# Kernel optimization log

Measured on AMD Instinct MI355X. Metric: run time of the kernel, lower is better.

The kernel has to match this reference:

```python
import jax, jax.numpy as jnp
import numpy as np
import math

HIDDEN = 1024
HEADS = 16

def setup_inputs() -> dict:
    key = jax.random.key(0)
    k1, k2, k3 = jax.random.split(key, 3)
    B, T, C = 4, 2048, HIDDEN
    x = jax.random.normal(k1, (B, T, C), dtype=jnp.float32)
    w_qkv = jax.random.normal(k2, (C, 3 * C), dtype=jnp.float32) * (1.0 / math.sqrt(C))
    b_qkv = jnp.zeros((3 * C,), dtype=jnp.float32)
    w_out = jax.random.normal(k3, (C, C), dtype=jnp.float32) * (1.0 / math.sqrt(C))
    b_out = jnp.zeros((C,), dtype=jnp.float32)
    return {"x": x, "w_qkv": w_qkv, "b_qkv": b_qkv, "w_out": w_out, "b_out": b_out}

def reference(x, w_qkv, b_qkv, w_out, b_out):
    B, T, C = x.shape
    H = HEADS
    D = C // H  # head dim
    qkv = x @ w_qkv + b_qkv  # [B,T,3C]
    q, k, v = jnp.split(qkv, 3, axis=2)
    # [B,T,C] -> [B,H,T,D]
    q = q.reshape(B, T, H, D).transpose(0, 2, 1, 3)
    k = k.reshape(B, T, H, D).transpose(0, 2, 1, 3)
    v = v.reshape(B, T, H, D).transpose(0, 2, 1, 3)
    scale = 1.0 / math.sqrt(D)
    logits = jnp.einsum('bhqd,bhkd->bhqk', q, k) * scale  # [B,H,T,T]
    causal = jnp.tril(jnp.ones((T, T), dtype=bool))
    logits = jnp.where(causal[None, None, :, :], logits, -jnp.inf)
    probs = jax.nn.softmax(logits, axis=-1)
    out = jnp.einsum('bhqk,bhkd->bhqd', probs, v)  # [B,H,T,D]
    out = out.transpose(0, 2, 1, 3).reshape(B, T, C)
    return out @ w_out + b_out
```

## Files before the change

kernel.cpp:

```cpp
#include <hip/hip_runtime.h>
#include <hip/hip_bf16.h>

#define C_DIM  1024
#define NHEAD  16
#define DHEAD  64
#define T_LEN  2048
#define B_SZ   4
#define M_ROWS (B_SZ * T_LEN)
#define QKV_N  (3 * C_DIM)

typedef __bf16 bf16x8 __attribute__((ext_vector_type(8)));
typedef float  f32x4  __attribute__((ext_vector_type(4)));
typedef unsigned short ushort8_t __attribute__((ext_vector_type(8)));
typedef unsigned int   uint4_t   __attribute__((ext_vector_type(4)));
typedef short          short4_t  __attribute__((ext_vector_type(4)));

#if __has_builtin(__builtin_amdgcn_mfma_f32_16x16x16bf16_1k)
#define HAVE_MFMA_X16 1
#else
#define HAVE_MFMA_X16 0
#endif

__device__ __forceinline__ unsigned short f2bf(float f) {
    union { float f; unsigned int u; } v; v.f = f;
    unsigned int r = v.u + 0x7FFFu + ((v.u >> 16) & 1u);
    return (unsigned short)(r >> 16);
}

__device__ __forceinline__ bf16x8 as_bf16x8(ushort8_t u) {
    return __builtin_bit_cast(bf16x8, u);
}

__device__ __forceinline__ f32x4 mfma16(bf16x8 a, bf16x8 b, f32x4 c) {
    return __builtin_amdgcn_mfma_f32_16x16x32_bf16(a, b, c, 0, 0, 0);
}

#define GLL16(gsrc, ldst) __builtin_amdgcn_global_load_lds( \
    (const __attribute__((address_space(1))) void*)(gsrc),  \
    (__attribute__((address_space(3))) void*)(ldst), 16, 0, 0)

__device__ __forceinline__ int xcd_remap(int id, int nwg) {
    const int q = nwg >> 3, r = nwg & 7;
    const int xcd = id & 7, off = id >> 3;
    return (xcd < r) ? (xcd * (q + 1) + off) : (r * (q + 1) + (xcd - r) * q + off);
}

__global__ void k_convert(const float* __restrict__ in, unsigned short* __restrict__ out, int n4) {
    int i = blockIdx.x * blockDim.x + threadIdx.x;
    if (i >= n4) return;
    const float4 v = ((const float4*)in)[i];
    unsigned int lo = (unsigned int)f2bf(v.x) | ((unsigned int)f2bf(v.y) << 16);
    unsigned int hi = (unsigned int)f2bf(v.z) | ((unsigned int)f2bf(v.w) << 16);
    ((uint2*)out)[i] = make_uint2(lo, hi);
}

__global__ void k_transpose_bf16(const float* __restrict__ w, unsigned short* __restrict__ wT,
                                 int K, int N) {
    __shared__ float tile[32][33];
    const int n0 = blockIdx.x * 32, k0 = blockIdx.y * 32;
    const int tx = threadIdx.x, ty = threadIdx.y;
    for (int i = 0; i < 32; i += 8)
        tile[ty + i][tx] = w[(size_t)(k0 + ty + i) * N + (n0 + tx)];
    __syncthreads();
    for (int i = 0; i < 32; i += 8)
        wT[(size_t)(n0 + ty + i) * K + (k0 + tx)] = f2bf(tile[tx][ty + i]);
}

__global__ void k_transpose_v(const unsigned short* __restrict__ qkv,
                              unsigned short* __restrict__ vtg) {
    __shared__ unsigned short tile[32][33];
    const int tt = blockIdx.x;
    const int dy = blockIdx.y;
    const int bh = dy >> 1, dtile = dy & 1;
    const int b = bh >> 4, h = bh & 15;
    const int t0 = tt * 32, d0 = dtile * 32;
    const int tx = threadIdx.x, ty = threadIdx.y;
    const unsigned short* src = qkv + (size_t)b * T_LEN * QKV_N + 2 * C_DIM + h * DHEAD + d0;
    for (int i = 0; i < 32; i += 8)
        tile[ty + i][tx] = src[(size_t)(t0 + ty + i) * QKV_N + tx];
    __syncthreads();
    unsigned short* dst = vtg + ((size_t)bh * DHEAD + d0) * T_LEN + t0;
    for (int i = 0; i < 32; i += 8)
        dst[(size_t)(ty + i) * T_LEN + tx] = tile[tx][ty + i];
}

template<int BF16_OUT>
__global__ __launch_bounds__(256) void k_gemm(const unsigned short* __restrict__ A,
                       const unsigned short* __restrict__ Bt,
                       const float* __restrict__ bias,
                       void* __restrict__ C,
                       unsigned short* __restrict__ vtg,
                       int M, int N, int K) {
    __shared__ unsigned short As[128][64];
    __shared__ unsigned short Bs[128][64];

    const int tid  = threadIdx.x;
    const int lane = tid & 63;
    const int wv   = tid >> 6;
    const int wm = wv >> 1, wn = wv & 1;

    const int nwg = gridDim.x * gridDim.y;
    const int wg  = xcd_remap(blockIdx.y * gridDim.x + blockIdx.x, nwg);
    const int bx = wg % gridDim.x, by = wg / gridDim.x;
    const int m0 = by * 128;
    const int n0 = bx * 128;
    const int lr = lane & 15, lg = lane >> 4;

    f32x4 acc[4][4];
#pragma unroll
    for (int i = 0; i < 4; i++)
#pragma unroll
        for (int j = 0; j < 4; j++) acc[i][j] = (f32x4){0.f, 0.f, 0.f, 0.f};

    const int gr = lane >> 3;
    const int gc = 8 * ((lane & 7) ^ gr);

    for (int kt = 0; kt < K; kt += 64) {
        __syncthreads();
#pragma unroll
        for (int j = 0; j < 4; j++) {
            const int row = 32 * wv + 8 * j;
            GLL16(A  + (size_t)(m0 + row + gr) * K + kt + gc, &As[row][0]);
            GLL16(Bt + (size_t)(n0 + row + gr) * K + kt + gc, &Bs[row][0]);
        }
        __syncthreads();

#pragma unroll
        for (int s = 0; s < 2; s++) {
            const int cb = (s * 64 + lg * 16) ^ ((lr & 7) << 4);
            bf16x8 af[4], bfr[4];
#pragma unroll
            for (int i = 0; i < 4; i++)
                af[i] = as_bf16x8(*(const ushort8_t*)((const char*)&As[wm * 64 + i * 16 + lr][0] + cb));
#pragma unroll
            for (int j = 0; j < 4; j++)
                bfr[j] = as_bf16x8(*(const ushort8_t*)((const char*)&Bs[wn * 64 + j * 16 + lr][0] + cb));
#pragma unroll
            for (int i = 0; i < 4; i++)
#pragma unroll
                for (int j = 0; j < 4; j++)
                    acc[i][j] = mfma16(af[i], bfr[j], acc[i][j]);
        }
    }

    const bool isV = (vtg != nullptr) && (n0 >= 2 * C_DIM);
#pragma unroll
    for (int i = 0; i < 4; i++) {
#pragma unroll
        for (int j = 0; j < 4; j++) {
            const int col = n0 + wn * 64 + j * 16 + lr;
            const float bv = bias ? bias[col] : 0.f;
            if (isV) {
                const int dcol = col - 2 * C_DIM;
                const int hh = dcol >> 6, dd = dcol & 63;
                const int row0 = m0 + wm * 64 + i * 16 + lg * 4;
                const int bb = row0 >> 11, t0 = row0 & (T_LEN - 1);
                const unsigned int p0 = (unsigned int)f2bf(acc[i][j][0] + bv)
                                      | ((unsigned int)f2bf(acc[i][j][1] + bv) << 16);
                const unsigned int p1 = (unsigned int)f2bf(acc[i][j][2] + bv)
                                      | ((unsigned int)f2bf(acc[i][j][3] + bv) << 16);
                *(uint2*)&vtg[(((size_t)(bb * 16 + hh)) * 64 + dd) * T_LEN + t0] = make_uint2(p0, p1);
            } else {
#pragma unroll
                for (int r = 0; r < 4; r++) {
                    const int row = m0 + wm * 64 + i * 16 + lg * 4 + r;
                    const float v = acc[i][j][r] + bv;
                    if (BF16_OUT)
                        ((unsigned short*)C)[(size_t)row * N + col] = f2bf(v);
                    else
                        ((float*)C)[(size_t)row * N + col] = v;
                }
            }
        }
    }
}

#define KS_OFF(B_, ROW_) (((B_) << 13) + ((ROW_) << 7))
#define VS_OFF(B_, ROW_) (16384 + ((B_) << 13) + ((ROW_) << 7))
#define SCALE2 0.180336880f
__global__ __launch_bounds__(256, 4) void k_attn(const unsigned short* __restrict__ qkv,
                                                 const unsigned short* __restrict__ vtg,
                                                 unsigned short* __restrict__ out) {
    __shared__ __align__(16) char asmem[32768];

    const int blk = xcd_remap(blockIdx.x, B_SZ * NHEAD * 16);
    const int pr = blk & 15;
    const int h  = (blk >> 4) & 15;
    const int b  = blk >> 8;
    const int bh = b * 16 + h;

    const int tid  = threadIdx.x;
    const int lane = tid & 63;
    const int w    = tid >> 6;
    const int lr = lane & 15, lg = lane >> 4;
    const int gr = lane >> 3;
    const int gc = 8 * ((lane & 7) ^ gr);
    const int ra = w * 16;

    const size_t base = (size_t)b * T_LEN * QKV_N + (size_t)h * DHEAD;
    const unsigned short* Qp = qkv + base;
    const unsigned short* Kp = qkv + base + C_DIM;
    const unsigned short* Vt = vtg + (size_t)bh * DHEAD * T_LEN;

    int buf = 0;
    for (int t = 0; t < 2; t++) {
        const int qt = (t == 0) ? pr : (31 - pr);
        const int qw = qt * 64 + w * 16;
        const int qg = qw + lr;
        const int R  = qt + 1;

        bf16x8 qf[2];
#pragma unroll
        for (int s = 0; s < 2; s++)
            qf[s] = as_bf16x8(*(const ushort8_t*)&Qp[(size_t)(qw + lr) * QKV_N + s * 32 + lg * 8]);

        f32x4 o[4];
#pragma unroll
        for (int f = 0; f < 4; f++) o[f] = (f32x4){0.f, 0.f, 0.f, 0.f};
        float lp = 0.f;

        GLL16(Kp + (size_t)(ra + gr) * QKV_N + gc,          asmem + KS_OFF(buf, ra));
        GLL16(Kp + (size_t)(ra + 8 + gr) * QKV_N + gc,      asmem + KS_OFF(buf, ra + 8));
        GLL16(Vt + (size_t)(ra + gr) * T_LEN + gc,          asmem + VS_OFF(buf, ra));
        GLL16(Vt + (size_t)(ra + 8 + gr) * T_LEN + gc,      asmem + VS_OFF(buf, ra + 8));

        for (int r = 0; r < R; ++r) {
            const int kb = r * 64;

            asm volatile("s_waitcnt vmcnt(0)" ::: "memory");
            __builtin_amdgcn_s_barrier();
            __builtin_amdgcn_sched_barrier(0);

            if (r + 1 < R) {
                const int kn = kb + 64;
                GLL16(Kp + (size_t)(kn + ra + gr) * QKV_N + gc,     asmem + KS_OFF(buf ^ 1, ra));
                GLL16(Kp + (size_t)(kn + ra + 8 + gr) * QKV_N + gc, asmem + KS_OFF(buf ^ 1, ra + 8));
                GLL16(Vt + (size_t)(ra + gr) * T_LEN + kn + gc,     asmem + VS_OFF(buf ^ 1, ra));
                GLL16(Vt + (size_t)(ra + 8 + gr) * T_LEN + kn + gc, asmem + VS_OFF(buf ^ 1, ra + 8));
            }

            f32x4 s4[4];
            __builtin_amdgcn_s_setprio(1);
#pragma unroll
            for (int f = 0; f < 4; f++) {
                const int row = f * 16 + lr;
                const bf16x8 kf0 = as_bf16x8(*(const ushort8_t*)
                    (asmem + KS_OFF(buf, row) + ((lg * 16) ^ ((lr & 7) << 4))));
                const bf16x8 kf1 = as_bf16x8(*(const ushort8_t*)
                    (asmem + KS_OFF(buf, row) + ((64 + lg * 16) ^ ((lr & 7) << 4))));
                f32x4 s = (f32x4){0.f, 0.f, 0.f, 0.f};
                s = mfma16(kf0, qf[0], s);
                s = mfma16(kf1, qf[1], s);
                s4[f] = s;
            }
            __builtin_amdgcn_s_setprio(0);

            const bool last = (r == R - 1);
            unsigned int pb[4][2];
#pragma unroll
            for (int f = 0; f < 4; f++) {
                unsigned short hh[4];
#pragma unroll
                for (int rr = 0; rr < 4; rr++) {
                    float sv = fminf(s4[f][rr] * SCALE2, 72.f);
                    if (last) {
                        const int kg = kb + f * 16 + lg * 4 + rr;
                        if (kg > qg) sv = -1e30f;
                    }
                    const float e = __builtin_amdgcn_exp2f(sv);
                    lp += e;
                    hh[rr] = __builtin_bit_cast(unsigned short, (__bf16)e);
                }
                pb[f][0] = (unsigned int)hh[0] | ((unsigned int)hh[1] << 16);
                pb[f][1] = (unsigned int)hh[2] | ((unsigned int)hh[3] << 16);
            }

            __builtin_amdgcn_s_setprio(1);
#pragma unroll
            for (int kg = 0; kg < 4; kg++) {
#if HAVE_MFMA_X16
                const short4_t pbv = __builtin_bit_cast(short4_t,
                    make_uint2(pb[kg][0], pb[kg][1]));
#else
                uint4_t pw;
                pw.x = pb[kg][0]; pw.y = pb[kg][1]; pw.z = 0u; pw.w = 0u;
                const bf16x8 pbv8 = __builtin_bit_cast(bf16x8, pw);
#endif
#pragma unroll
                for (int fd = 0; fd < 4; fd++) {
                    const int drow = fd * 16 + lr;
                    const uint2 va = *(const uint2*)(asmem + VS_OFF(buf, drow) +
                                     ((kg * 32 + lg * 8) ^ ((lr & 7) << 4)));
#if HAVE_MFMA_X16
                    o[fd] = __builtin_amdgcn_mfma_f32_16x16x16bf16_1k(
                        __builtin_bit_cast(short4_t, va), pbv, o[fd], 0, 0, 0);
#else
                    uint4_t vw;
                    vw.x = va.x; vw.y = va.y; vw.z = va.x; vw.w = va.y;
                    o[fd] = mfma16(__builtin_bit_cast(bf16x8, vw), pbv8, o[fd]);
#endif
                }
            }
            __builtin_amdgcn_s_setprio(0);

            buf ^= 1;
        }

        lp += __shfl_xor(lp, 16, 64);
        lp += __shfl_xor(lp, 32, 64);
        const float inv = 1.f / lp;

#pragma unroll
        for (int fd = 0; fd < 4; fd++)
#pragma unroll
            for (int rr = 0; rr < 4; rr++) {
                const int d = fd * 16 + lg * 4 + rr;
                out[((size_t)b * T_LEN + qw + lr) * C_DIM + h * DHEAD + d] =
                    f2bf(o[fd][rr] * inv);
            }
    }
}

extern "C" void kernel_launch(void* const* d_in, const int* in_sizes, int n_in,
                              void* d_out, int out_size, void* d_ws, size_t ws_size,
                              hipStream_t stream) {
    const float* x      = (const float*)d_in[0];
    const float* w_qkv  = (const float*)d_in[1];
    const float* b_qkv  = (const float*)d_in[2];
    const float* w_out  = (const float*)d_in[3];
    const float* b_out  = (const float*)d_in[4];
    float* out = (float*)d_out;

    char* ws = (char*)d_ws;
    unsigned short* xb    = (unsigned short*)(ws);
    unsigned short* wqkvT = (unsigned short*)(ws + 16777216);
    unsigned short* woutT = (unsigned short*)(ws + 16777216 + 6291456);
    unsigned short* qkv   = (unsigned short*)(ws + 25165824);
    unsigned short* attn  = (unsigned short*)(ws + 75497472);

    const size_t VTG_OFF = 92274688ull;
    const bool fused_vt = (ws_size >= VTG_OFF + 16777216ull);
    unsigned short* vtg = fused_vt ? (unsigned short*)(ws + VTG_OFF)
                                   : (unsigned short*)(ws);

    {
        const int n4 = M_ROWS * C_DIM / 4;
        k_convert<<<(n4 + 255) / 256, 256, 0, stream>>>(x, xb, n4);
    }
    k_transpose_bf16<<<dim3(QKV_N / 32, C_DIM / 32), dim3(32, 8), 0, stream>>>(w_qkv, wqkvT, C_DIM, QKV_N);
    k_transpose_bf16<<<dim3(C_DIM / 32, C_DIM / 32), dim3(32, 8), 0, stream>>>(w_out, woutT, C_DIM, C_DIM);
    k_gemm<1><<<dim3(QKV_N / 128, M_ROWS / 128), 256, 0, stream>>>(
        xb, wqkvT, b_qkv, qkv, fused_vt ? vtg : nullptr, M_ROWS, QKV_N, C_DIM);
    if (!fused_vt)
        k_transpose_v<<<dim3(T_LEN / 32, 64 * 2), dim3(32, 8), 0, stream>>>(qkv, vtg);
    k_attn<<<B_SZ * NHEAD * 16, 256, 0, stream>>>(qkv, vtg, attn);
    k_gemm<0><<<dim3(C_DIM / 128, M_ROWS / 128), 256, 0, stream>>>(
        attn, woutT, b_out, out, nullptr, M_ROWS, C_DIM, C_DIM);
}
```

Measured before the change: 169.0 us.

## Replace QKV GEMM with 256x256-tile, 4-stage LDS pipelined kernel

Adds a 512-thread GEMM with 256x256 output tiles for the QKV projection. It uses a 4-slot, 128KB dynamic-LDS ring filled by direct global-to-LDS loads, interleaved with MFMA phases under s_setprio and explicit vmcnt waits. The aim is to hide global load latency and raise per-block data reuse compared with the 128x128 single-buffered kernel. The cost is a large LDS footprint that limits occupancy to one block per CU, and a grid of only 384 blocks on 256 CUs, which leaves the last wave underfilled. The old kernel keeps only the plain output path, used by the output projection.

Result: slower. 174.4 us (+3.2%).

```diff
diff --git a/kernel.cpp b/kernel.cpp
--- a/kernel.cpp
+++ b/kernel.cpp
@@ -84,12 +84,173 @@
         dst[(size_t)(ty + i) * T_LEN + tx] = tile[tx][ty + i];
 }
 
+#define SLOT_A(u) (((u) & 3) * 16384)
+#define SLOT_B(u) (65536 + ((u) & 3) * 16384)
+__device__ __forceinline__ void stage_unit(const unsigned short* __restrict__ M,
+                                           int K, int row0, int kcol0,
+                                           char* lds_slot, int wv, int lane) {
+#pragma unroll
+    for (int j = 0; j < 2; j++) {
+        const int row = wv * 32 + j * 16 + (lane >> 2);
+        const int sc  = 8 * ((lane & 3) ^ ((wv * 16 + j * 8 + (lane >> 3)) & 3));
+        GLL16(M + (size_t)(row0 + row) * K + kcol0 + sc,
+              lds_slot + wv * 2048 + j * 1024);
+    }
+}
+
+__global__ __launch_bounds__(512) void k_gemm256p(const unsigned short* __restrict__ A,
+                       const unsigned short* __restrict__ Bt,
+                       const float* __restrict__ bias,
+                       unsigned short* __restrict__ C,
+                       unsigned short* __restrict__ vtg,
+                       int M, int N, int K) {
+    extern __shared__ char smem[];
+
+    const int tid  = threadIdx.x;
+    const int lane = tid & 63;
+    const int wv   = tid >> 6;
+    const int wm = wv >> 2, wn = wv & 3;
+    const int lr = lane & 15, lg = lane >> 4;
+    const int rpos = (lg ^ ((lr >> 1) & 3)) << 4;
+
+    const int gx  = gridDim.x;
+    const int nwg = gx * gridDim.y;
+    const int wg  = xcd_remap(blockIdx.y * gx + blockIdx.x, nwg);
+    const int bx = wg % gx, by = wg / gx;
+    const int m0 = by * 256, n0 = bx * 256;
+    const int NT = K >> 6;
+
+    f32x4 acc[8][4];
+#pragma unroll
+    for (int mi = 0; mi < 8; mi++)
+#pragma unroll
+        for (int ni = 0; ni < 4; ni++) acc[mi][ni] = (f32x4){0.f, 0.f, 0.f, 0.f};
+
+    stage_unit(A,  K, m0, 0,  smem + SLOT_A(0), wv, lane);
+    stage_unit(Bt, K, n0, 0,  smem + SLOT_B(0), wv, lane);
+    stage_unit(A,  K, m0, 32, smem + SLOT_A(1), wv, lane);
+    stage_unit(Bt, K, n0, 32, smem + SLOT_B(1), wv, lane);
+    if (NT > 1) {
+        stage_unit(A,  K, m0, 64, smem + SLOT_A(2), wv, lane);
+        stage_unit(Bt, K, n0, 64, smem + SLOT_B(2), wv, lane);
+        asm volatile("s_waitcnt vmcnt(4)" ::: "memory");
+    } else {
+        asm volatile("s_waitcnt vmcnt(0)" ::: "memory");
+    }
+    __builtin_amdgcn_s_barrier();
+    __builtin_amdgcn_sched_barrier(0);
+
+    const int arow = wm * 128 + lr;
+    const int brow = wn * 64 + lr;
+
+    for (int t = 0; t < NT; ++t) {
+        const char* sA0 = smem + SLOT_A(2 * t);
+        const char* sA1 = smem + SLOT_A(2 * t + 1);
+        const char* sB0 = smem + SLOT_B(2 * t);
+        const char* sB1 = smem + SLOT_B(2 * t + 1);
+
+        bf16x8 af[4], bfr[4];
+
+        if (t + 1 < NT)
+            stage_unit(A, K, m0, (t + 1) * 64 + 32, smem + SLOT_A(2 * t + 3), wv, lane);
+#pragma unroll
+        for (int ni = 0; ni < 4; ni++)
+            bfr[ni] = as_bf16x8(*(const ushort8_t*)(sB0 + (brow + ni * 16) * 64 + rpos));
+#pragma unroll
+        for (int mi = 0; mi < 4; mi++)
+            af[mi] = as_bf16x8(*(const ushort8_t*)(sA0 + (arow + mi * 16) * 64 + rpos));
+        __builtin_amdgcn_s_setprio(1);
+#pragma unroll
+        for (int mi = 0; mi < 4; mi++)
+#pragma unroll
+            for (int ni = 0; ni < 4; ni++)
+                acc[mi][ni] = mfma16(af[mi], bfr[ni], acc[mi][ni]);
+        __builtin_amdgcn_s_setprio(0);
+
+        if (t + 1 < NT)
+            stage_unit(Bt, K, n0, (t + 1) * 64 + 32, smem + SLOT_B(2 * t + 3), wv, lane);
+#pragma unroll
+        for (int mi = 0; mi < 4; mi++)
+            af[mi] = as_bf16x8(*(const ushort8_t*)(sA0 + (arow + (4 + mi) * 16) * 64 + rpos));
+        __builtin_amdgcn_s_setprio(1);
+#pragma unroll
+        for (int mi = 0; mi < 4; mi++)
+#pragma unroll
+            for (int ni = 0; ni < 4; ni++)
+                acc[4 + mi][ni] = mfma16(af[mi], bfr[ni], acc[4 + mi][ni]);
+        __builtin_amdgcn_s_setprio(0);
+        __builtin_amdgcn_s_barrier();
+        __builtin_amdgcn_sched_barrier(0);
+
+        if (t + 2 < NT)
+            stage_unit(A, K, m0, (t + 2) * 64, smem + SLOT_A(2 * t + 4), wv, lane);
+#pragma unroll
+        for (int ni = 0; ni < 4; ni++)
+            bfr[ni] = as_bf16x8(*(const ushort8_t*)(sB1 + (brow + ni * 16) * 64 + rpos));
+#pragma unroll
+        for (int mi = 0; mi < 4; mi++)
+            af[mi] = as_bf16x8(*(const ushort8_t*)(sA1 + (arow + mi * 16) * 64 + rpos));
+        __builtin_amdgcn_s_setprio(1);
+#pragma unroll
+        for (int mi = 0; mi < 4; mi++)
+#pragma unroll
+            for (int ni = 0; ni < 4; ni++)
+                acc[mi][ni] = mfma16(af[mi], bfr[ni], acc[mi][ni]);
+        __builtin_amdgcn_s_setprio(0);
+
+        if (t + 2 < NT)
+            stage_unit(Bt, K, n0, (t + 2) * 64, smem + SLOT_B(2 * t + 4), wv, lane);
+#pragma unroll
+        for (int mi = 0; mi < 4; mi++)
+            af[mi] = as_bf16x8(*(const ushort8_t*)(sA1 + (arow + (4 + mi) * 16) * 64 + rpos));
+        __builtin_amdgcn_s_setprio(1);
+#pragma unroll
+        for (int mi = 0; mi < 4; mi++)
+#pragma unroll
+            for (int ni = 0; ni < 4; ni++)
+                acc[4 + mi][ni] = mfma16(af[mi], bfr[ni], acc[4 + mi][ni]);
+        __builtin_amdgcn_s_setprio(0);
+
+        if (t + 2 < NT) {
+            asm volatile("s_waitcnt vmcnt(4)" ::: "memory");
+        } else if (t + 1 < NT) {
+            asm volatile("s_waitcnt vmcnt(0)" ::: "memory");
+        }
+        __builtin_amdgcn_s_barrier();
+        __builtin_amdgcn_sched_barrier(0);
+    }
+
+    const bool isV = (vtg != nullptr) && (n0 >= 2 * C_DIM);
+#pragma unroll
+    for (int mi = 0; mi < 8; mi++) {
+        const int row0 = m0 + wm * 128 + mi * 16 + lg * 4;
+#pragma unroll
+        for (int ni = 0; ni < 4; ni++) {
+            const int col = n0 + wn * 64 + ni * 16 + lr;
+            const float bv = bias ? bias[col] : 0.f;
+            if (isV) {
+                const int dcol = col - 2 * C_DIM;
+                const int hh = dcol >> 6, dd = dcol & 63;
+                const int bb = row0 >> 11, t0 = row0 & (T_LEN - 1);
+                const unsigned int p0 = (unsigned int)f2bf(acc[mi][ni][0] + bv)
+                                      | ((unsigned int)f2bf(acc[mi][ni][1] + bv) << 16);
+                const unsigned int p1 = (unsigned int)f2bf(acc[mi][ni][2] + bv)
+                                      | ((unsigned int)f2bf(acc[mi][ni][3] + bv) << 16);
+                *(uint2*)&vtg[(((size_t)(bb * 16 + hh)) * 64 + dd) * T_LEN + t0] = make_uint2(p0, p1);
+            } else {
+#pragma unroll
+                for (int rr = 0; rr < 4; rr++)
+                    C[(size_t)(row0 + rr) * N + col] = f2bf(acc[mi][ni][rr] + bv);
+            }
+        }
+    }
+}
+
 template<int BF16_OUT>
 __global__ __launch_bounds__(256) void k_gemm(const unsigned short* __restrict__ A,
                        const unsigned short* __restrict__ Bt,
                        const float* __restrict__ bias,
                        void* __restrict__ C,
-                       unsigned short* __restrict__ vtg,
                        int M, int N, int K) {
     __shared__ unsigned short As[128][64];
     __shared__ unsigned short Bs[128][64];
@@ -143,33 +304,20 @@
         }
     }
 
-    const bool isV = (vtg != nullptr) && (n0 >= 2 * C_DIM);
 #pragma unroll
     for (int i = 0; i < 4; i++) {
 #pragma unroll
         for (int j = 0; j < 4; j++) {
             const int col = n0 + wn * 64 + j * 16 + lr;
             const float bv = bias ? bias[col] : 0.f;
-            if (isV) {
-                const int dcol = col - 2 * C_DIM;
-                const int hh = dcol >> 6, dd = dcol & 63;
-                const int row0 = m0 + wm * 64 + i * 16 + lg * 4;
-                const int bb = row0 >> 11, t0 = row0 & (T_LEN - 1);
-                const unsigned int p0 = (unsigned int)f2bf(acc[i][j][0] + bv)
-                                      | ((unsigned int)f2bf(acc[i][j][1] + bv) << 16);
-                const unsigned int p1 = (unsigned int)f2bf(acc[i][j][2] + bv)
-                                      | ((unsigned int)f2bf(acc[i][j][3] + bv) << 16);
-                *(uint2*)&vtg[(((size_t)(bb * 16 + hh)) * 64 + dd) * T_LEN + t0] = make_uint2(p0, p1);
-            } else {
-#pragma unroll
-                for (int r = 0; r < 4; r++) {
-                    const int row = m0 + wm * 64 + i * 16 + lg * 4 + r;
-                    const float v = acc[i][j][r] + bv;
-                    if (BF16_OUT)
-                        ((unsigned short*)C)[(size_t)row * N + col] = f2bf(v);
-                    else
-                        ((float*)C)[(size_t)row * N + col] = v;
-                }
+#pragma unroll
+            for (int r = 0; r < 4; r++) {
+                const int row = m0 + wm * 64 + i * 16 + lg * 4 + r;
+                const float v = acc[i][j][r] + bv;
+                if (BF16_OUT)
+                    ((unsigned short*)C)[(size_t)row * N + col] = f2bf(v);
+                else
+                    ((float*)C)[(size_t)row * N + col] = v;
             }
         }
     }
@@ -349,11 +497,11 @@
     }
     k_transpose_bf16<<<dim3(QKV_N / 32, C_DIM / 32), dim3(32, 8), 0, stream>>>(w_qkv, wqkvT, C_DIM, QKV_N);
     k_transpose_bf16<<<dim3(C_DIM / 32, C_DIM / 32), dim3(32, 8), 0, stream>>>(w_out, woutT, C_DIM, C_DIM);
-    k_gemm<1><<<dim3(QKV_N / 128, M_ROWS / 128), 256, 0, stream>>>(
+    k_gemm256p<<<dim3(QKV_N / 256, M_ROWS / 256), 512, 131072, stream>>>(
         xb, wqkvT, b_qkv, qkv, fused_vt ? vtg : nullptr, M_ROWS, QKV_N, C_DIM);
     if (!fused_vt)
         k_transpose_v<<<dim3(T_LEN / 32, 64 * 2), dim3(32, 8), 0, stream>>>(qkv, vtg);
     k_attn<<<B_SZ * NHEAD * 16, 256, 0, stream>>>(qkv, vtg, attn);
     k_gemm<0><<<dim3(C_DIM / 128, M_ROWS / 128), 256, 0, stream>>>(
-        attn, woutT, b_out, out, nullptr, M_ROWS, C_DIM, C_DIM);
-}
+        attn, woutT, b_out, out, M_ROWS, C_DIM, C_DIM);
+}
```
